# Kernel tuning notes

Measured on AMD Instinct MI355X. Metric: run time of the kernel, lower is better.

The kernel has to match this reference:

```python
import jax, jax.numpy as jnp
import numpy as np

# Module hyperparameters (init_kwargs)
TOP_K = 0.15          # fraction of pixels kept per row when step_percent=1
IGNORE_INDEX = 255

B, K, N, H, W = 8, 3, 8, 384, 384


def setup_inputs() -> dict:
    key = jax.random.key(0)
    k1, k2 = jax.random.split(key)
    # log-probabilities over K classes (nll_loss expects log-probs)
    logits = jax.random.normal(k1, (B, K, N, H, W), dtype=jnp.float32)
    inp = jax.nn.log_softmax(logits, axis=1)
    target = jax.random.randint(k2, (B, N, H, W), 0, K, dtype=jnp.int32)
    return {"input": inp, "target": target, "step_percent": 1}


def reference(input, target, step_percent):
    b, k, n, h, w = input.shape
    P = h * w
    x = input.reshape(b * n, k, P)           # (BN, K, P)
    t = target.reshape(b * n, P)             # (BN, P)

    # per-pixel NLL with ignore_index (ignored pixels contribute 0)
    mask = t != IGNORE_INDEX
    t_safe = jnp.where(mask, t, 0)
    nll = -jnp.take_along_axis(x, t_safe[:, None, :], axis=1)[:, 0, :]  # (BN, P)
    nll = jnp.where(mask, nll, jnp.zeros((), nll.dtype))

    # static k: step_percent is a Python scalar in the original forward
    sp = min(float(step_percent), 1.0)
    n_top_k = int(sp * TOP_K * P + (1.0 - sp) * P)

    top_k_loss, _ = jax.lax.top_k(nll, n_top_k)  # (BN, n_top_k)
    return jnp.mean(top_k_loss)
```

## Files before the change

kernel.cpp:

```cpp
#include <hip/hip_runtime.h>

#define BN    64
#define KCLS  3
#define PPIX  147456
#define NB1   4096
#define NB3   128
#define CAP   8192

#define BPR    32
#define F4PB   (PPIX / 4 / BPR)
#define PXB    (F4PB * 4)

#define SCOPE __HIP_MEMORY_SCOPE_AGENT

static const size_t OFF_NLL  = 0;
static const size_t OFF_CAND = OFF_NLL + (size_t)BN * PPIX * 4;
static const size_t OFF_GH   = OFF_CAND + (size_t)BN * CAP * 4;
static const size_t OFF_CCNT = OFF_GH + (size_t)BN * NB1 * 4;
static const size_t OFF_SS   = OFF_CCNT + 256;
static const size_t OFF_ACC  = OFF_SS + 512;
static const size_t OFF_DONE = OFF_ACC + 8;
static const size_t ZERO_END = OFF_DONE + 8;
static const size_t OFF_B1   = ZERO_END;
static const size_t OFF_R1   = ZERO_END + 256;

__device__ __forceinline__ unsigned topk_count(const int* sp_ptr) {
    double sp = (double)sp_ptr[0];
    if (sp > 1.0) sp = 1.0;
    return (unsigned)(sp * 0.15 * (double)PPIX + (1.0 - sp) * (double)PPIX);
}

__device__ __forceinline__ float sel_nll(int t, float a, float b, float c) {
    float lp = (t == 0) ? a : ((t == 1) ? b : ((t == 2) ? c : 0.0f));
    return fmaxf(-lp, 0.0f);
}

__global__ __launch_bounds__(256) void k_hist1(
    const float* __restrict__ in, const int* __restrict__ tgt,
    float* __restrict__ nll, unsigned* __restrict__ cnt1)
{
    __shared__ unsigned lc[NB1];
    const int tid = threadIdx.x;
    for (int i = tid; i < NB1; i += 256) lc[i] = 0u;
    __syncthreads();

    const int row   = blockIdx.x / BPR;
    const int chunk = blockIdx.x % BPR;
    const float4* p0 = (const float4*)(in + (size_t)row * KCLS * PPIX);
    const float4* p1 = p0 + PPIX / 4;
    const float4* p2 = p1 + PPIX / 4;
    const int4*   t4 = (const int4*)(tgt + (size_t)row * PPIX);
    float4*       n4 = (float4*)(nll + (size_t)row * PPIX);
    const int base = chunk * F4PB;
    const bool tail = (tid < (F4PB - 4 * 256));

    int idx_c = base + tid;
    int4   t_c = t4[idx_c];
    float4 a_c = p0[idx_c];
    float4 b_c = p1[idx_c];
    float4 c_c = p2[idx_c];

    #pragma unroll
    for (int j = 0; j < 4; ++j) {
        int idx_n = 0;
        int4 t_n; float4 a_n, b_n, c_n;
        const bool have_next = (j < 3) || tail;
        if (have_next) {
            idx_n = base + (j + 1) * 256 + tid;
            t_n = t4[idx_n];
            a_n = p0[idx_n];
            b_n = p1[idx_n];
            c_n = p2[idx_n];
        }

        float4 v;
        v.x = sel_nll(t_c.x, a_c.x, b_c.x, c_c.x);
        v.y = sel_nll(t_c.y, a_c.y, b_c.y, c_c.y);
        v.z = sel_nll(t_c.z, a_c.z, b_c.z, c_c.z);
        v.w = sel_nll(t_c.w, a_c.w, b_c.w, c_c.w);
        n4[idx_c] = v;
        atomicAdd(&lc[__float_as_uint(v.x) >> 19], 1u);
        atomicAdd(&lc[__float_as_uint(v.y) >> 19], 1u);
        atomicAdd(&lc[__float_as_uint(v.z) >> 19], 1u);
        atomicAdd(&lc[__float_as_uint(v.w) >> 19], 1u);

        idx_c = idx_n; t_c = t_n; a_c = a_n; b_c = b_n; c_c = c_n;
    }

    if (tail) {
        float4 v;
        v.x = sel_nll(t_c.x, a_c.x, b_c.x, c_c.x);
        v.y = sel_nll(t_c.y, a_c.y, b_c.y, c_c.y);
        v.z = sel_nll(t_c.z, a_c.z, b_c.z, c_c.z);
        v.w = sel_nll(t_c.w, a_c.w, b_c.w, c_c.w);
        n4[idx_c] = v;
        atomicAdd(&lc[__float_as_uint(v.x) >> 19], 1u);
        atomicAdd(&lc[__float_as_uint(v.y) >> 19], 1u);
        atomicAdd(&lc[__float_as_uint(v.z) >> 19], 1u);
        atomicAdd(&lc[__float_as_uint(v.w) >> 19], 1u);
    }
    __syncthreads();

    unsigned* gc = cnt1 + (size_t)row * NB1;
    for (int i = tid; i < NB1; i += 256) {
        const unsigned cc = lc[i];
        if (cc) atomicAdd(&gc[i], cc);
    }
}

__global__ __launch_bounds__(256) void k_scompact(
    const float* __restrict__ nll, const unsigned* __restrict__ ghist,
    const int* __restrict__ sp, float* __restrict__ cand,
    int* __restrict__ ccnt, double* __restrict__ st_S,
    int* __restrict__ st_b, int* __restrict__ st_r)
{
    __shared__ float  stage[PXB];
    __shared__ double wsum[4];
    __shared__ int s_b1, s_r1, lcnt, gbase;

    const int tid   = threadIdx.x;
    const int row   = blockIdx.x / BPR;
    const int chunk = blockIdx.x % BPR;

    {
        unsigned* csum = (unsigned*)stage;
        const unsigned* c = ghist + (size_t)row * NB1;
        unsigned cl[16]; unsigned cacc = 0;
        const int base = tid * 16;
        #pragma unroll
        for (int i = 0; i < 16; ++i) {
            cl[i] = c[NB1 - 1 - (base + i)];
            cacc += cl[i];
        }
        csum[tid] = cacc;
        __syncthreads();
        for (int off = 1; off < 256; off <<= 1) {
            unsigned t2 = (tid >= off) ? csum[tid - off] : 0u;
            __syncthreads();
            csum[tid] += t2;
            __syncthreads();
        }
        const unsigned k = topk_count(sp);
        unsigned cum = tid ? csum[tid - 1] : 0u;
        #pragma unroll
        for (int i = 0; i < 16; ++i) {
            const unsigned cb = cl[i];
            if (cum < k && cum + cb >= k) {
                s_b1 = NB1 - 1 - (base + i);
                s_r1 = (int)(k - cum);
            }
            cum += cb;
        }
        if (tid == 0) lcnt = 0;
    }
    __syncthreads();
    if (chunk == 0 && tid == 0) {
        st_b[row] = s_b1;
        st_r[row] = s_r1;
    }

    const unsigned b1 = (unsigned)s_b1;
    const unsigned lo = b1 << 19;
    const unsigned hi = (b1 + 1u) << 19;
    const float4* n4 = (const float4*)(nll + (size_t)row * PPIX);
    const int base = chunk * F4PB;

    double acc = 0.0;
    #pragma unroll
    for (int j = 0; j < 5; ++j) {
        if (j == 4 && tid >= (F4PB - 4 * 256)) break;
        const float4 f = n4[base + j * 256 + tid];
        const float vv[4] = {f.x, f.y, f.z, f.w};
        #pragma unroll
        for (int q = 0; q < 4; ++q) {
            const unsigned u = __float_as_uint(vv[q]);
            if (u >= hi) {
                acc += (double)vv[q];
            } else if (u >= lo) {
                const int s = atomicAdd(&lcnt, 1);
                stage[s] = vv[q];
            }
        }
    }

    #pragma unroll
    for (int off = 32; off > 0; off >>= 1) acc += __shfl_down(acc, off, 64);
    if ((tid & 63) == 0) wsum[tid >> 6] = acc;
    __syncthreads();
    if (tid == 0) {
        atomicAdd(&st_S[row], (wsum[0] + wsum[1]) + (wsum[2] + wsum[3]));
        gbase = atomicAdd(&ccnt[row], lcnt);
    }
    __syncthreads();

    const int n = lcnt, gb = gbase;
    float* cr = cand + (size_t)row * CAP;
    for (int i = tid; i < n; i += 256) {
        const int pos = gb + i;
        if (pos < CAP) cr[pos] = stage[i];
    }
}

__global__ __launch_bounds__(256) void k_resolve(
    const float* __restrict__ cand, const int* __restrict__ ccnt,
    const int* __restrict__ st_b1, const int* __restrict__ st_r1,
    const double* __restrict__ st_S, const int* __restrict__ sp,
    double* __restrict__ accum, unsigned* __restrict__ done,
    float* __restrict__ out)
{
    __shared__ unsigned lc[NB1];
    __shared__ float    ls[NB1];
    __shared__ unsigned csum[256];
    __shared__ double   ssum[256];
    __shared__ int sb2, sr2;
    __shared__ double sS2;

    const int row = blockIdx.x, tid = threadIdx.x;
    int n = ccnt[row]; if (n > CAP) n = CAP;
    const float* cv = cand + (size_t)row * CAP;

    for (int i = tid; i < NB1; i += 256) { lc[i] = 0u; ls[i] = 0.0f; }
    __syncthreads();
    for (int i = tid; i < n; i += 256) {
        const float v = cv[i];
        const unsigned key = (__float_as_uint(v) >> 7) & 0xFFFu;
        atomicAdd(&lc[key], 1u);
        atomicAdd(&ls[key], v);
    }
    __syncthreads();

    unsigned cl[16]; float slv[16];
    unsigned cacc = 0; double sacc = 0.0;
    const int base = tid * 16;
    #pragma unroll
    for (int i = 0; i < 16; ++i) {
        const int bin = NB1 - 1 - (base + i);
        cl[i]  = lc[bin];
        slv[i] = ls[bin];
        cacc += cl[i];
        sacc += (double)slv[i];
    }
    csum[tid] = cacc; ssum[tid] = sacc;
    __syncthreads();
    for (int off = 1; off < 256; off <<= 1) {
        unsigned cv2 = 0; double sv = 0.0;
        if (tid >= off) { cv2 = csum[tid - off]; sv = ssum[tid - off]; }
        __syncthreads();
        csum[tid] += cv2; ssum[tid] += sv;
        __syncthreads();
    }
    const unsigned k = (unsigned)st_r1[row];
    unsigned cum = tid ? csum[tid - 1] : 0u;
    double   sS  = tid ? ssum[tid - 1] : 0.0;
    #pragma unroll
    for (int i = 0; i < 16; ++i) {
        const unsigned cb = cl[i];
        if (cum < k && cum + cb >= k) {
            sb2 = NB1 - 1 - (base + i);
            sr2 = (int)(k - cum);
            sS2 = sS;
        }
        cum += cb;
        sS  += (double)slv[i];
    }
    __syncthreads();

    const unsigned pref = ((unsigned)st_b1[row] << 12) | (unsigned)sb2;
    if (tid < NB3) { lc[tid] = 0u; ls[tid] = 0.0f; }
    __syncthreads();
    for (int i = tid; i < n; i += 256) {
        const float v = cv[i];
        const unsigned bits = __float_as_uint(v);
        if ((bits >> 7) == pref) {
            atomicAdd(&lc[bits & 0x7Fu], 1u);
            atomicAdd(&ls[bits & 0x7Fu], v);
        }
    }
    __syncthreads();
    if (tid == 0) {
        const unsigned k3 = (unsigned)sr2;
        unsigned cum3 = 0, r3 = 0; int b3 = 0; double S3 = 0.0;
        for (int bin = NB3 - 1; bin >= 0; --bin) {
            const unsigned cb = lc[bin];
            if (cum3 < k3 && cum3 + cb >= k3) { b3 = bin; r3 = k3 - cum3; break; }
            cum3 += cb;
            S3   += (double)ls[bin];
        }
        const float tval = __uint_as_float((pref << 7) | (unsigned)b3);
        const double total = st_S[row] + sS2 + S3 + (double)r3 * (double)tval;
        atomicAdd(accum, total);
        __threadfence();
        const unsigned ticket =
            __hip_atomic_fetch_add(done, 1u, __ATOMIC_ACQ_REL, SCOPE);
        if (ticket == BN - 1) {
            const double a2 =
                __hip_atomic_load(accum, __ATOMIC_RELAXED, SCOPE);
            out[0] = (float)(a2 / ((double)BN * (double)topk_count(sp)));
        }
    }
}

extern "C" void kernel_launch(void* const* d_in, const int* in_sizes, int n_in,
                              void* d_out, int out_size, void* d_ws, size_t ws_size,
                              hipStream_t stream)
{
    (void)in_sizes; (void)n_in; (void)out_size; (void)ws_size;
    const float* in  = (const float*)d_in[0];
    const int*   tgt = (const int*)d_in[1];
    const int*   sp  = (const int*)d_in[2];

    char* ws = (char*)d_ws;
    float*    nll   = (float*)(ws + OFF_NLL);
    float*    cand  = (float*)(ws + OFF_CAND);
    unsigned* ghist = (unsigned*)(ws + OFF_GH);
    int*      ccnt  = (int*)(ws + OFF_CCNT);
    double*   st_S  = (double*)(ws + OFF_SS);
    double*   accum = (double*)(ws + OFF_ACC);
    unsigned* done  = (unsigned*)(ws + OFF_DONE);
    int*      st_b1 = (int*)(ws + OFF_B1);
    int*      st_r1 = (int*)(ws + OFF_R1);

    hipMemsetAsync(ws + OFF_GH, 0, ZERO_END - OFF_GH, stream);

    k_hist1   <<<BN * BPR, 256, 0, stream>>>(in, tgt, nll, ghist);
    k_scompact<<<BN * BPR, 256, 0, stream>>>(nll, ghist, sp, cand, ccnt, st_S,
                                             st_b1, st_r1);
    k_resolve <<<BN,       256, 0, stream>>>(cand, ccnt, st_b1, st_r1, st_S,
                                             sp, accum, done, (float*)d_out);
}
```

Measured before the change: 246.4 us.

## Rebalance radix-select bins and halve blocks per row with wider chunks

Changes the three-level radix split from 13/12/7 bits to 12/12/8 bits, shrinking the first-pass histogram to 2048 bins and doubling the candidate buffer capacity. Halves blocks per row so each block handles nine full float4 iterations with no tail, and drops the manual software prefetch. Global histogram flushes now use 64-bit atomics that carry two bin counts each. This reduces per-block histogram zeroing and global atomic traffic and lowers block count, but coarser first-level bins pass more candidates to the compaction and resolve stages and overflow risk moves to the larger CAP.

```diff
diff --git a/kernel.cpp b/kernel.cpp
--- a/kernel.cpp
+++ b/kernel.cpp
@@ -3,11 +3,13 @@
 #define BN    64
 #define KCLS  3
 #define PPIX  147456
-#define NB1   4096
-#define NB3   128
-#define CAP   8192
-
-#define BPR    32
+#define NB1L  2048
+#define SH1   20
+#define NB2   4096
+#define NB3   256
+#define CAP   16384
+
+#define BPR    16
 #define F4PB   (PPIX / 4 / BPR)
 #define PXB    (F4PB * 4)
 
@@ -16,7 +18,7 @@
 static const size_t OFF_NLL  = 0;
 static const size_t OFF_CAND = OFF_NLL + (size_t)BN * PPIX * 4;
 static const size_t OFF_GH   = OFF_CAND + (size_t)BN * CAP * 4;
-static const size_t OFF_CCNT = OFF_GH + (size_t)BN * NB1 * 4;
+static const size_t OFF_CCNT = OFF_GH + (size_t)BN * NB1L * 4;
 static const size_t OFF_SS   = OFF_CCNT + 256;
 static const size_t OFF_ACC  = OFF_SS + 512;
 static const size_t OFF_DONE = OFF_ACC + 8;
@@ -39,9 +41,9 @@
     const float* __restrict__ in, const int* __restrict__ tgt,
     float* __restrict__ nll, unsigned* __restrict__ cnt1)
 {
-    __shared__ unsigned lc[NB1];
+    __shared__ unsigned lc[NB1L];
     const int tid = threadIdx.x;
-    for (int i = tid; i < NB1; i += 256) lc[i] = 0u;
+    for (int i = tid; i < NB1L; i += 256) lc[i] = 0u;
     __syncthreads();
 
     const int row   = blockIdx.x / BPR;
@@ -52,59 +54,35 @@
     const int4*   t4 = (const int4*)(tgt + (size_t)row * PPIX);
     float4*       n4 = (float4*)(nll + (size_t)row * PPIX);
     const int base = chunk * F4PB;
-    const bool tail = (tid < (F4PB - 4 * 256));
-
-    int idx_c = base + tid;
-    int4   t_c = t4[idx_c];
-    float4 a_c = p0[idx_c];
-    float4 b_c = p1[idx_c];
-    float4 c_c = p2[idx_c];
-
-    #pragma unroll
-    for (int j = 0; j < 4; ++j) {
-        int idx_n = 0;
-        int4 t_n; float4 a_n, b_n, c_n;
-        const bool have_next = (j < 3) || tail;
-        if (have_next) {
-            idx_n = base + (j + 1) * 256 + tid;
-            t_n = t4[idx_n];
-            a_n = p0[idx_n];
-            b_n = p1[idx_n];
-            c_n = p2[idx_n];
-        }
-
+
+    #pragma unroll
+    for (int j = 0; j < 9; ++j) {
+        const int idx = base + j * 256 + tid;
+        const int4   t = t4[idx];
+        const float4 a = p0[idx];
+        const float4 b = p1[idx];
+        const float4 c = p2[idx];
         float4 v;
-        v.x = sel_nll(t_c.x, a_c.x, b_c.x, c_c.x);
-        v.y = sel_nll(t_c.y, a_c.y, b_c.y, c_c.y);
-        v.z = sel_nll(t_c.z, a_c.z, b_c.z, c_c.z);
-        v.w = sel_nll(t_c.w, a_c.w, b_c.w, c_c.w);
-        n4[idx_c] = v;
-        atomicAdd(&lc[__float_as_uint(v.x) >> 19], 1u);
-        atomicAdd(&lc[__float_as_uint(v.y) >> 19], 1u);
-        atomicAdd(&lc[__float_as_uint(v.z) >> 19], 1u);
-        atomicAdd(&lc[__float_as_uint(v.w) >> 19], 1u);
-
-        idx_c = idx_n; t_c = t_n; a_c = a_n; b_c = b_n; c_c = c_n;
-    }
-
-    if (tail) {
-        float4 v;
-        v.x = sel_nll(t_c.x, a_c.x, b_c.x, c_c.x);
-        v.y = sel_nll(t_c.y, a_c.y, b_c.y, c_c.y);
-        v.z = sel_nll(t_c.z, a_c.z, b_c.z, c_c.z);
-        v.w = sel_nll(t_c.w, a_c.w, b_c.w, c_c.w);
-        n4[idx_c] = v;
-        atomicAdd(&lc[__float_as_uint(v.x) >> 19], 1u);
-        atomicAdd(&lc[__float_as_uint(v.y) >> 19], 1u);
-        atomicAdd(&lc[__float_as_uint(v.z) >> 19], 1u);
-        atomicAdd(&lc[__float_as_uint(v.w) >> 19], 1u);
-    }
-    __syncthreads();
-
-    unsigned* gc = cnt1 + (size_t)row * NB1;
-    for (int i = tid; i < NB1; i += 256) {
-        const unsigned cc = lc[i];
-        if (cc) atomicAdd(&gc[i], cc);
+        v.x = sel_nll(t.x, a.x, b.x, c.x);
+        v.y = sel_nll(t.y, a.y, b.y, c.y);
+        v.z = sel_nll(t.z, a.z, b.z, c.z);
+        v.w = sel_nll(t.w, a.w, b.w, c.w);
+        n4[idx] = v;
+        atomicAdd(&lc[__float_as_uint(v.x) >> SH1], 1u);
+        atomicAdd(&lc[__float_as_uint(v.y) >> SH1], 1u);
+        atomicAdd(&lc[__float_as_uint(v.z) >> SH1], 1u);
+        atomicAdd(&lc[__float_as_uint(v.w) >> SH1], 1u);
+    }
+    __syncthreads();
+
+    unsigned long long* gc8 =
+        (unsigned long long*)(cnt1 + (size_t)row * NB1L);
+    for (int i = tid; i < NB1L / 2; i += 256) {
+        const unsigned lo = lc[2 * i];
+        const unsigned hi = lc[2 * i + 1];
+        if (lo | hi)
+            atomicAdd(&gc8[i], (unsigned long long)lo |
+                               ((unsigned long long)hi << 32));
     }
 }
 
@@ -124,12 +102,12 @@
 
     {
         unsigned* csum = (unsigned*)stage;
-        const unsigned* c = ghist + (size_t)row * NB1;
-        unsigned cl[16]; unsigned cacc = 0;
-        const int base = tid * 16;
+        const unsigned* c = ghist + (size_t)row * NB1L;
+        unsigned cl[8]; unsigned cacc = 0;
+        const int base = tid * 8;
         #pragma unroll
-        for (int i = 0; i < 16; ++i) {
-            cl[i] = c[NB1 - 1 - (base + i)];
+        for (int i = 0; i < 8; ++i) {
+            cl[i] = c[NB1L - 1 - (base + i)];
             cacc += cl[i];
         }
         csum[tid] = cacc;
@@ -143,10 +121,10 @@
         const unsigned k = topk_count(sp);
         unsigned cum = tid ? csum[tid - 1] : 0u;
         #pragma unroll
-        for (int i = 0; i < 16; ++i) {
+        for (int i = 0; i < 8; ++i) {
             const unsigned cb = cl[i];
             if (cum < k && cum + cb >= k) {
-                s_b1 = NB1 - 1 - (base + i);
+                s_b1 = NB1L - 1 - (base + i);
                 s_r1 = (int)(k - cum);
             }
             cum += cb;
@@ -160,15 +138,14 @@
     }
 
     const unsigned b1 = (unsigned)s_b1;
-    const unsigned lo = b1 << 19;
-    const unsigned hi = (b1 + 1u) << 19;
+    const unsigned lo = b1 << SH1;
+    const unsigned hi = (b1 + 1u) << SH1;
     const float4* n4 = (const float4*)(nll + (size_t)row * PPIX);
     const int base = chunk * F4PB;
 
     double acc = 0.0;
     #pragma unroll
-    for (int j = 0; j < 5; ++j) {
-        if (j == 4 && tid >= (F4PB - 4 * 256)) break;
+    for (int j = 0; j < 9; ++j) {
         const float4 f = n4[base + j * 256 + tid];
         const float vv[4] = {f.x, f.y, f.z, f.w};
         #pragma unroll
@@ -208,8 +185,8 @@
     double* __restrict__ accum, unsigned* __restrict__ done,
     float* __restrict__ out)
 {
-    __shared__ unsigned lc[NB1];
-    __shared__ float    ls[NB1];
+    __shared__ unsigned lc[NB2];
+    __shared__ float    ls[NB2];
     __shared__ unsigned csum[256];
     __shared__ double   ssum[256];
     __shared__ int sb2, sr2;
@@ -219,11 +196,11 @@
     int n = ccnt[row]; if (n > CAP) n = CAP;
     const float* cv = cand + (size_t)row * CAP;
 
-    for (int i = tid; i < NB1; i += 256) { lc[i] = 0u; ls[i] = 0.0f; }
+    for (int i = tid; i < NB2; i += 256) { lc[i] = 0u; ls[i] = 0.0f; }
     __syncthreads();
     for (int i = tid; i < n; i += 256) {
         const float v = cv[i];
-        const unsigned key = (__float_as_uint(v) >> 7) & 0xFFFu;
+        const unsigned key = (__float_as_uint(v) >> 8) & 0xFFFu;
         atomicAdd(&lc[key], 1u);
         atomicAdd(&ls[key], v);
     }
@@ -234,7 +211,7 @@
     const int base = tid * 16;
     #pragma unroll
     for (int i = 0; i < 16; ++i) {
-        const int bin = NB1 - 1 - (base + i);
+        const int bin = NB2 - 1 - (base + i);
         cl[i]  = lc[bin];
         slv[i] = ls[bin];
         cacc += cl[i];
@@ -256,7 +233,7 @@
     for (int i = 0; i < 16; ++i) {
         const unsigned cb = cl[i];
         if (cum < k && cum + cb >= k) {
-            sb2 = NB1 - 1 - (base + i);
+            sb2 = NB2 - 1 - (base + i);
             sr2 = (int)(k - cum);
             sS2 = sS;
         }
@@ -271,9 +248,9 @@
     for (int i = tid; i < n; i += 256) {
         const float v = cv[i];
         const unsigned bits = __float_as_uint(v);
-        if ((bits >> 7) == pref) {
-            atomicAdd(&lc[bits & 0x7Fu], 1u);
-            atomicAdd(&ls[bits & 0x7Fu], v);
+        if ((bits >> 8) == pref) {
+            atomicAdd(&lc[bits & 0xFFu], 1u);
+            atomicAdd(&ls[bits & 0xFFu], v);
         }
     }
     __syncthreads();
@@ -286,7 +263,7 @@
             cum3 += cb;
             S3   += (double)ls[bin];
         }
-        const float tval = __uint_as_float((pref << 7) | (unsigned)b3);
+        const float tval = __uint_as_float((pref << 8) | (unsigned)b3);
         const double total = st_S[row] + sS2 + S3 + (double)r3 * (double)tval;
         atomicAdd(accum, total);
         __threadfence();
```

New measurement: 262.0 us. +6.4%, slower.
